# Kernel tuning notes

Hardware: AMD Instinct MI355X
Metric: run time of the kernel (lower is better)

The kernel has to match this reference:

```python
import jax, jax.numpy as jnp
import numpy as np

DIM = 256
RDIM = 64  # max(256 // 4, 16)
SCALE = RDIM ** (-0.5)
BN_EPS = 1e-5


def conv1x1(x, w):
    # x: (B, Cin, H, W), w: (Cout, Cin) -> (B, Cout, H, W)
    return jnp.einsum('bchw,oc->bohw', x, w)


def dot_attn(q, k, v):
    # q: (B, rdim, H, W); k: (B, rdim, H, W); v: (B, C, H, W)
    B, C, H, W = v.shape
    q_flat = q.reshape(B, -1, H * W).transpose(0, 2, 1)   # (B, N, rdim)
    k_flat = k.reshape(B, -1, H * W)                       # (B, rdim, N)
    v_flat = v.reshape(B, C, H * W).transpose(0, 2, 1)     # (B, N, C)
    attn = jax.nn.softmax(jnp.einsum('bnc,bcm->bnm', q_flat, k_flat) * SCALE, axis=-1)
    out = jnp.einsum('bnm,bmc->bnc', attn, v_flat)         # (B, N, C)
    return out.transpose(0, 2, 1).reshape(B, C, H, W)


def batchnorm2d(x, gamma, beta):
    # training-mode BN: stats over (B, H, W) per channel
    mean = jnp.mean(x, axis=(0, 2, 3), keepdims=True)
    var = jnp.var(x, axis=(0, 2, 3), keepdims=True)
    xn = (x - mean) * jax.lax.rsqrt(var + BN_EPS)
    return xn * gamma[None, :, None, None] + beta[None, :, None, None]


def setup_inputs() -> dict:
    key = jax.random.key(0)
    ks = jax.random.split(key, 12)
    B, H, W = 4, 64, 64
    s_q = 1.0 / np.sqrt(DIM)
    return {
        'wli_feat': jax.random.normal(ks[0], (B, DIM, H, W), jnp.float32),
        'nbi_aligned': jax.random.normal(ks[1], (B, DIM, H, W), jnp.float32),
        'w_q_wli': jax.random.normal(ks[2], (RDIM, DIM), jnp.float32) * s_q,
        'w_k_nbi': jax.random.normal(ks[3], (RDIM, DIM), jnp.float32) * s_q,
        'w_v_nbi': jax.random.normal(ks[4], (DIM, DIM), jnp.float32) * s_q,
        'w_q_nbi': jax.random.normal(ks[5], (RDIM, DIM), jnp.float32) * s_q,
        'w_k_wli': jax.random.normal(ks[6], (RDIM, DIM), jnp.float32) * s_q,
        'w_v_wli': jax.random.normal(ks[7], (DIM, DIM), jnp.float32) * s_q,
        'gamma_wli': jnp.ones((DIM,), jnp.float32),
        'beta_wli': jnp.zeros((DIM,), jnp.float32),
        'gamma_nbi': jnp.ones((DIM,), jnp.float32),
        'beta_nbi': jnp.zeros((DIM,), jnp.float32),
    }


def reference(wli_feat, nbi_aligned, w_q_wli, w_k_nbi, w_v_nbi, w_q_nbi, w_k_wli, w_v_wli,
              gamma_wli, beta_wli, gamma_nbi, beta_nbi):
    ctx_wli = dot_attn(conv1x1(wli_feat, w_q_wli), conv1x1(nbi_aligned, w_k_nbi),
                       conv1x1(nbi_aligned, w_v_nbi))
    enh_wli = batchnorm2d(wli_feat + ctx_wli, gamma_wli, beta_wli)
    ctx_nbi = dot_attn(conv1x1(nbi_aligned, w_q_nbi), conv1x1(wli_feat, w_k_wli),
                       conv1x1(wli_feat, w_v_wli))
    enh_nbi = batchnorm2d(nbi_aligned + ctx_nbi, gamma_nbi, beta_nbi)
    return enh_wli, enh_nbi
```

## Files before the change

kernel.cpp:

```cpp
#include <hip/hip_runtime.h>

#define N_TOK 4096
#define RD 64
#define CDIM 256

typedef __bf16 bf16x8 __attribute__((ext_vector_type(8)));
typedef float f32x4 __attribute__((ext_vector_type(4)));
typedef unsigned short u16;
typedef unsigned int u32;

__device__ __forceinline__ u16 f2bf(float f) {
  u32 u = __float_as_uint(f);
  u = (u + 0x7fffu + ((u >> 16) & 1u)) >> 16;
  return (u16)u;
}

__device__ __forceinline__ u32 pack2bf(float a, float b) {
  u16 ha = __builtin_bit_cast(u16, (__bf16)a);
  u16 hb = __builtin_bit_cast(u16, (__bf16)b);
  return (u32)ha | ((u32)hb << 16);
}

__device__ __forceinline__ f32x4 zero4() {
  f32x4 z = {0.f, 0.f, 0.f, 0.f};
  return z;
}

__global__ __launch_bounds__(256) void proj_kernel(
    const float* __restrict__ wli, const float* __restrict__ nbi,
    const float* __restrict__ wq0, const float* __restrict__ wk0,
    const float* __restrict__ wv0, const float* __restrict__ wq1,
    const float* __restrict__ wk1, const float* __restrict__ wv1,
    u16* __restrict__ Qb, u16* __restrict__ Kb, u16* __restrict__ Vb) {
  extern __shared__ char smem[];
  const int ntile = blockIdx.x, bb = blockIdx.y, pid = blockIdx.z;
  const int tid = threadIdx.x;
  const int w = tid >> 6, lane = tid & 63, g = lane >> 4, l15 = lane & 15;
  const int n0 = ntile * 64;

  const float* X;
  const float* W;
  u16* out;
  float scale = 1.f;
  int form, nchunk;
  switch (pid) {
    case 0: X = wli; W = wq0; out = Qb + (size_t)(0 + bb) * N_TOK * RD; scale = 0.125f; form = 1; nchunk = 1; break;
    case 1: X = nbi; W = wk0; out = Kb + (size_t)(0 + bb) * N_TOK * RD; form = 1; nchunk = 1; break;
    case 2: X = nbi; W = wv0; out = Vb + (size_t)(0 + bb) * CDIM * N_TOK; form = 2; nchunk = 4; break;
    case 3: X = nbi; W = wq1; out = Qb + (size_t)(4 + bb) * N_TOK * RD; scale = 0.125f; form = 1; nchunk = 1; break;
    case 4: X = wli; W = wk1; out = Kb + (size_t)(4 + bb) * N_TOK * RD; form = 1; nchunk = 1; break;
    default: X = wli; W = wv1; out = Vb + (size_t)(4 + bb) * CDIM * N_TOK; form = 2; nchunk = 4; break;
  }
  X += (size_t)bb * CDIM * N_TOK;

#pragma unroll
  for (int rep = 0; rep < 16; ++rep) {
    int idx = rep * 256 + tid;
    int c = idx >> 4;
    int nq = (idx & 15) * 4;
    float4 v = *(const float4*)(X + (size_t)c * N_TOK + n0 + nq);
    float vv[4] = {v.x, v.y, v.z, v.w};
#pragma unroll
    for (int k = 0; k < 4; ++k) {
      int row = nq + k;
      int addr = (row * 512 + c * 2) ^ ((row & 7) << 4);
      *(u16*)(smem + addr) = f2bf(vv[k] * scale);
    }
  }

  for (int oc = 0; oc < nchunk; ++oc) {
#pragma unroll
    for (int rep = 0; rep < 16; ++rep) {
      int idx = rep * 256 + tid;
      int o = idx >> 6;
      int c4 = (idx & 63) * 4;
      float4 v = *(const float4*)(W + (size_t)(oc * 64 + o) * CDIM + c4);
      ushort4 pk = {f2bf(v.x), f2bf(v.y), f2bf(v.z), f2bf(v.w)};
      int addr = 32768 + ((o * 512 + c4 * 2) ^ ((o & 7) << 4));
      *(ushort4*)(smem + addr) = pk;
    }
    __syncthreads();

    f32x4 acc[4];
#pragma unroll
    for (int ct = 0; ct < 4; ++ct) acc[ct] = zero4();
    const int arow = w * 16 + l15;
    const int abase = (form == 1) ? 0 : 32768;
    const int bbase = (form == 1) ? 32768 : 0;
#pragma unroll
    for (int kk = 0; kk < 8; ++kk) {
      int koff = kk * 64 + g * 16;
      bf16x8 af = *(const bf16x8*)(smem + abase + ((arow * 512 + koff) ^ ((arow & 7) << 4)));
#pragma unroll
      for (int ct = 0; ct < 4; ++ct) {
        int brow = ct * 16 + l15;
        bf16x8 bfr = *(const bf16x8*)(smem + bbase + ((brow * 512 + koff) ^ ((brow & 7) << 4)));
        acc[ct] = __builtin_amdgcn_mfma_f32_16x16x32_bf16(af, bfr, acc[ct], 0, 0, 0);
      }
    }
    if (form == 1) {
#pragma unroll
      for (int ct = 0; ct < 4; ++ct)
#pragma unroll
        for (int r = 0; r < 4; ++r)
          out[(size_t)(n0 + w * 16 + g * 4 + r) * RD + ct * 16 + l15] = f2bf(acc[ct][r]);
    } else {
#pragma unroll
      for (int ct = 0; ct < 4; ++ct)
#pragma unroll
        for (int r = 0; r < 4; ++r)
          out[(size_t)(oc * 64 + w * 16 + g * 4 + r) * N_TOK + n0 + ct * 16 + l15] = f2bf(acc[ct][r]);
    }
    __syncthreads();
  }
}

__global__ __launch_bounds__(256, 2) void attn_kernel(
    const u16* __restrict__ Qb, const u16* __restrict__ Kb,
    const u16* __restrict__ Vb, const float* __restrict__ x_wli,
    const float* __restrict__ x_nbi, float* __restrict__ y) {
  extern __shared__ char smem[];
  const int wgid = blockIdx.x;
  const int inst = wgid & 7;
  const int ntile = wgid >> 3;
  const int br = inst >> 2, bb = inst & 3;
  const int tid = threadIdx.x;
  const int w = tid >> 6, lane = tid & 63, g = lane >> 4, l15 = lane & 15;
  const u16* Q = Qb + (size_t)inst * N_TOK * RD + (size_t)ntile * 64 * RD;
  const u16* K = Kb + (size_t)inst * N_TOK * RD;
  const u16* Vt = Vb + (size_t)inst * CDIM * N_TOK;
  const float* xres = (br == 0 ? x_wli : x_nbi) + (size_t)bb * CDIM * N_TOK;
  float* yout = y + (size_t)inst * CDIM * N_TOK;

  bf16x8 qf[2];
  {
    const u16* qrow = Q + (w * 16 + l15) * RD;
    qf[0] = *(const bf16x8*)(qrow + g * 8);
    qf[1] = *(const bf16x8*)(qrow + 32 + g * 8);
  }
  f32x4 o_acc[16];
#pragma unroll
  for (int i = 0; i < 16; ++i) o_acc[i] = zero4();
  float m_ln = -1e30f, l_ln = 0.f;
  const float LOG2E = 1.44269504088896340736f;

#define STAGE_KV(kv0_, boff_)                                                    \
  {                                                                              \
    _Pragma("unroll") for (int rr = 0; rr < 2; ++rr) {                           \
      int s = w * 128 + rr * 64 + lane;                                          \
      int j = s >> 3, c16 = s & 7;                                               \
      const u16* gp = K + (size_t)((kv0_) + j) * RD + ((c16 ^ (j & 7)) * 8);     \
      char* lp = smem + (boff_) + (w * 128 + rr * 64) * 16;                      \
      __builtin_amdgcn_global_load_lds(                                          \
          (const __attribute__((address_space(1))) void*)gp,                     \
          (__attribute__((address_space(3))) void*)lp, 16, 0, 0);                \
    }                                                                            \
    _Pragma("unroll") for (int rr = 0; rr < 8; ++rr) {                           \
      int s = w * 512 + rr * 64 + lane;                                          \
      int c = s >> 3, c16 = s & 7;                                               \
      const u16* gp = Vt + (size_t)c * N_TOK + (kv0_) + ((c16 ^ (c & 7)) * 8);   \
      char* lp = smem + (boff_) + 8192 + (w * 512 + rr * 64) * 16;               \
      __builtin_amdgcn_global_load_lds(                                          \
          (const __attribute__((address_space(1))) void*)gp,                     \
          (__attribute__((address_space(3))) void*)lp, 16, 0, 0);                \
    }                                                                            \
  }

  STAGE_KV(0, 0);
  __syncthreads();

  for (int t = 0; t < 64; ++t) {
    const int kv0 = t * 64;
    const int bufOff = (t & 1) * 40960;
    if (t < 63) STAGE_KV(kv0 + 64, ((t + 1) & 1) * 40960);

    f32x4 s[4];
#pragma unroll
    for (int jt = 0; jt < 4; ++jt) {
      f32x4 acc = zero4();
#pragma unroll
      for (int kk = 0; kk < 2; ++kk) {
        int row = jt * 16 + l15;
        int addr = bufOff + ((row * 128 + kk * 64 + g * 16) ^ ((row & 7) << 4));
        bf16x8 kf = *(const bf16x8*)(smem + addr);
        acc = __builtin_amdgcn_mfma_f32_16x16x32_bf16(kf, qf[kk], acc, 0, 0, 0);
      }
      s[jt] = acc;
    }

    float mx = s[0][0];
#pragma unroll
    for (int jt = 0; jt < 4; ++jt)
#pragma unroll
      for (int r = 0; r < 4; ++r) mx = fmaxf(mx, s[jt][r]);
    mx = fmaxf(mx, __shfl_xor(mx, 16));
    mx = fmaxf(mx, __shfl_xor(mx, 32));
    if (!__all(mx - m_ln <= 8.f)) {
      float mnew = fmaxf(m_ln, mx);
      float corr = exp2f((m_ln - mnew) * LOG2E);
      m_ln = mnew;
      l_ln *= corr;
      float corrO[4];
#pragma unroll
      for (int r = 0; r < 4; ++r) corrO[r] = __shfl(corr, (lane & 48) | (g * 4 + r));
#pragma unroll
      for (int ct = 0; ct < 16; ++ct)
#pragma unroll
        for (int r = 0; r < 4; ++r) o_acc[ct][r] *= corrO[r];
    }
    float sum = 0.f;
#pragma unroll
    for (int jt = 0; jt < 4; ++jt)
#pragma unroll
      for (int r = 0; r < 4; ++r) {
        float p = exp2f((s[jt][r] - m_ln) * LOG2E);
        s[jt][r] = p;
        sum += p;
      }
    sum += __shfl_xor(sum, 16);
    sum += __shfl_xor(sum, 32);
    l_ln += sum;

    u32 pk[8];
#pragma unroll
    for (int jt = 0; jt < 4; ++jt) {
      pk[jt * 2] = pack2bf(s[jt][0], s[jt][1]);
      pk[jt * 2 + 1] = pack2bf(s[jt][2], s[jt][3]);
    }
    bf16x8 pf[2];
#pragma unroll
    for (int kk = 0; kk < 2; ++kk) {
      u32 wsel[4];
#pragma unroll
      for (int m = 0; m < 4; ++m) {
        int src = (2 * (g & 1) + (m >> 1)) * 16 + l15;
        u32 w0 = (u32)__shfl((int)pk[(2 * kk + 0) * 2 + (m & 1)], src);
        u32 w1 = (u32)__shfl((int)pk[(2 * kk + 1) * 2 + (m & 1)], src);
        wsel[m] = (g & 2) ? w1 : w0;
      }
      int4 pw = {(int)wsel[0], (int)wsel[1], (int)wsel[2], (int)wsel[3]};
      pf[kk] = __builtin_bit_cast(bf16x8, pw);
    }

    __builtin_amdgcn_s_setprio(1);
#pragma unroll
    for (int ct = 0; ct < 16; ++ct) {
      int c = ct * 16 + l15;
      int vb = bufOff + 8192;
      bf16x8 vf0 = *(const bf16x8*)(smem + vb + ((c * 128 + g * 16) ^ ((c & 7) << 4)));
      bf16x8 vf1 = *(const bf16x8*)(smem + vb + ((c * 128 + 64 + g * 16) ^ ((c & 7) << 4)));
      o_acc[ct] = __builtin_amdgcn_mfma_f32_16x16x32_bf16(pf[0], vf0, o_acc[ct], 0, 0, 0);
      o_acc[ct] = __builtin_amdgcn_mfma_f32_16x16x32_bf16(pf[1], vf1, o_acc[ct], 0, 0, 0);
    }
    __builtin_amdgcn_s_setprio(0);
    __syncthreads();
  }

  float rl = 1.f / l_ln;
  float rlO[4];
#pragma unroll
  for (int r = 0; r < 4; ++r) rlO[r] = __shfl(rl, (lane & 48) | (g * 4 + r));
  const int nbase = ntile * 64 + w * 16;
#pragma unroll
  for (int ct = 0; ct < 16; ++ct) {
    int c = ct * 16 + l15;
#pragma unroll
    for (int r = 0; r < 4; ++r) {
      size_t idx = (size_t)c * N_TOK + nbase + g * 4 + r;
      yout[idx] = xres[idx] + o_acc[ct][r] * rlO[r];
    }
  }
#undef STAGE_KV
}

__global__ __launch_bounds__(256) void bn_stats_kernel(const float* __restrict__ y,
                                                       float* __restrict__ stats) {
  const int idx = blockIdx.x;
  const int br = idx >> 8, c = idx & 255;
  const float* base = y + (size_t)br * 4 * CDIM * N_TOK + (size_t)c * N_TOK;
  float s1 = 0.f, s2 = 0.f;
#pragma unroll
  for (int bb = 0; bb < 4; ++bb) {
    const float* p = base + (size_t)bb * CDIM * N_TOK;
    for (int off = threadIdx.x * 4; off < N_TOK; off += 1024) {
      float4 v = *(const float4*)(p + off);
      s1 += v.x + v.y + v.z + v.w;
      s2 += v.x * v.x + v.y * v.y + v.z * v.z + v.w * v.w;
    }
  }
#pragma unroll
  for (int msk = 1; msk < 64; msk <<= 1) {
    s1 += __shfl_xor(s1, msk);
    s2 += __shfl_xor(s2, msk);
  }
  __shared__ float a1[4], a2[4];
  const int wv = threadIdx.x >> 6, ln = threadIdx.x & 63;
  if (ln == 0) { a1[wv] = s1; a2[wv] = s2; }
  __syncthreads();
  if (threadIdx.x == 0) {
    float t1 = a1[0] + a1[1] + a1[2] + a1[3];
    float t2 = a2[0] + a2[1] + a2[2] + a2[3];
    float mean = t1 * (1.f / 16384.f);
    float var = t2 * (1.f / 16384.f) - mean * mean;
    stats[idx] = mean;
    stats[512 + idx] = rsqrtf(var + 1e-5f);
  }
}

__global__ __launch_bounds__(256) void bn_apply_kernel(
    const float* __restrict__ y, const float* __restrict__ stats,
    const float* __restrict__ g0, const float* __restrict__ b0,
    const float* __restrict__ g1, const float* __restrict__ b1,
    float* __restrict__ out) {
  size_t i4 = (size_t)blockIdx.x * 256 + threadIdx.x;
  int br = (int)(i4 >> 20);
  int c = (int)(i4 >> 10) & 255;
  float mean = stats[br * 256 + c];
  float rstd = stats[512 + br * 256 + c];
  float ga = (br ? g1 : g0)[c];
  float be = (br ? b1 : b0)[c];
  float a = rstd * ga;
  float4 v = *(const float4*)(y + i4 * 4);
  v.x = (v.x - mean) * a + be;
  v.y = (v.y - mean) * a + be;
  v.z = (v.z - mean) * a + be;
  v.w = (v.w - mean) * a + be;
  *(float4*)(out + i4 * 4) = v;
}

extern "C" void kernel_launch(void* const* d_in, const int* in_sizes, int n_in,
                              void* d_out, int out_size, void* d_ws, size_t ws_size,
                              hipStream_t stream) {
  const float* wli = (const float*)d_in[0];
  const float* nbi = (const float*)d_in[1];
  const float* wq0 = (const float*)d_in[2];
  const float* wk0 = (const float*)d_in[3];
  const float* wv0 = (const float*)d_in[4];
  const float* wq1 = (const float*)d_in[5];
  const float* wk1 = (const float*)d_in[6];
  const float* wv1 = (const float*)d_in[7];
  const float* g0 = (const float*)d_in[8];
  const float* b0 = (const float*)d_in[9];
  const float* g1 = (const float*)d_in[10];
  const float* b1 = (const float*)d_in[11];

  char* ws = (char*)d_ws;
  u16* Qb = (u16*)(ws + 0);
  u16* Kb = (u16*)(ws + 4194304);
  u16* Vb = (u16*)(ws + 8388608);
  float* y = (float*)(ws + 25165824);
  float* stats = (float*)(ws + 58720256);

  proj_kernel<<<dim3(64, 4, 6), 256, 65536, stream>>>(wli, nbi, wq0, wk0, wv0,
                                                      wq1, wk1, wv1, Qb, Kb, Vb);
  attn_kernel<<<dim3(512), 256, 81920, stream>>>(Qb, Kb, Vb, wli, nbi, y);
  bn_stats_kernel<<<dim3(512), 256, 0, stream>>>(y, stats);
  bn_apply_kernel<<<dim3(8192), 256, 0, stream>>>(y, stats, g0, b0, g1, b1,
                                                  (float*)d_out);
}
```

Before: 301.7 us.

## Split attention waves into 2x2 query/channel tiles and drop P shuffles via 16x16x16 MFMA

Each wave now handles 32 queries and 128 output channels instead of 16 queries and 256 channels. K fragments are reused across two query tiles and V fragments across both query tiles. The P matrix is fed directly into 16x16x16 bf16 MFMAs from the QK accumulator layout, which removes the cross-lane shuffle repacking. It also adds explicit vmcnt drains before the barriers so the async LDS loads are complete, at the cost of duplicated QK and softmax work per wave pair and possibly less overlap.

After: 342.7 us. 1.14x slower.

```diff
diff --git a/kernel.cpp b/kernel.cpp
--- a/kernel.cpp
+++ b/kernel.cpp
@@ -8,6 +8,8 @@
 typedef float f32x4 __attribute__((ext_vector_type(4)));
 typedef unsigned short u16;
 typedef unsigned int u32;
+typedef u32 u32x2 __attribute__((ext_vector_type(2)));
+typedef short s16x4 __attribute__((ext_vector_type(4)));
 
 __device__ __forceinline__ u16 f2bf(float f) {
   u32 u = __float_as_uint(f);
@@ -25,6 +27,19 @@
   f32x4 z = {0.f, 0.f, 0.f, 0.f};
   return z;
 }
+
+__device__ __forceinline__ f32x4 mfma16bf(u32x2 a, u32x2 b, f32x4 c) {
+#if __has_builtin(__builtin_amdgcn_mfma_f32_16x16x16bf16_1k)
+  return __builtin_amdgcn_mfma_f32_16x16x16bf16_1k(
+      __builtin_bit_cast(s16x4, a), __builtin_bit_cast(s16x4, b), c, 0, 0, 0);
+#else
+  f32x4 d = c;
+  asm("v_mfma_f32_16x16x16_bf16 %0, %1, %2, %0" : "+v"(d) : "v"(a), "v"(b));
+  return d;
+#endif
+}
+
+#define DRAIN_VMCNT() asm volatile("s_waitcnt vmcnt(0)" ::: "memory")
 
 __global__ __launch_bounds__(256) void proj_kernel(
     const float* __restrict__ wli, const float* __restrict__ nbi,
@@ -126,29 +141,33 @@
   const int br = inst >> 2, bb = inst & 3;
   const int tid = threadIdx.x;
   const int w = tid >> 6, lane = tid & 63, g = lane >> 4, l15 = lane & 15;
+  const int wq = w >> 1, wc = w & 1;
   const u16* Q = Qb + (size_t)inst * N_TOK * RD + (size_t)ntile * 64 * RD;
   const u16* K = Kb + (size_t)inst * N_TOK * RD;
   const u16* Vt = Vb + (size_t)inst * CDIM * N_TOK;
   const float* xres = (br == 0 ? x_wli : x_nbi) + (size_t)bb * CDIM * N_TOK;
   float* yout = y + (size_t)inst * CDIM * N_TOK;
 
-  bf16x8 qf[2];
-  {
-    const u16* qrow = Q + (w * 16 + l15) * RD;
-    qf[0] = *(const bf16x8*)(qrow + g * 8);
-    qf[1] = *(const bf16x8*)(qrow + 32 + g * 8);
-  }
-  f32x4 o_acc[16];
-#pragma unroll
-  for (int i = 0; i < 16; ++i) o_acc[i] = zero4();
-  float m_ln = -1e30f, l_ln = 0.f;
+  bf16x8 qf[2][2];
+#pragma unroll
+  for (int qt = 0; qt < 2; ++qt) {
+    const u16* qrow = Q + (wq * 32 + qt * 16 + l15) * RD;
+    qf[qt][0] = *(const bf16x8*)(qrow + g * 8);
+    qf[qt][1] = *(const bf16x8*)(qrow + 32 + g * 8);
+  }
+  f32x4 o_acc[2][8];
+#pragma unroll
+  for (int qt = 0; qt < 2; ++qt)
+#pragma unroll
+    for (int ct = 0; ct < 8; ++ct) o_acc[qt][ct] = zero4();
+  float m_ln[2] = {-1e30f, -1e30f}, l_ln[2] = {0.f, 0.f};
   const float LOG2E = 1.44269504088896340736f;
 
 #define STAGE_KV(kv0_, boff_)                                                    \
   {                                                                              \
     _Pragma("unroll") for (int rr = 0; rr < 2; ++rr) {                           \
-      int s = w * 128 + rr * 64 + lane;                                          \
-      int j = s >> 3, c16 = s & 7;                                               \
+      int s_ = w * 128 + rr * 64 + lane;                                         \
+      int j = s_ >> 3, c16 = s_ & 7;                                             \
       const u16* gp = K + (size_t)((kv0_) + j) * RD + ((c16 ^ (j & 7)) * 8);     \
       char* lp = smem + (boff_) + (w * 128 + rr * 64) * 16;                      \
       __builtin_amdgcn_global_load_lds(                                          \
@@ -156,8 +175,8 @@
           (__attribute__((address_space(3))) void*)lp, 16, 0, 0);                \
     }                                                                            \
     _Pragma("unroll") for (int rr = 0; rr < 8; ++rr) {                           \
-      int s = w * 512 + rr * 64 + lane;                                          \
-      int c = s >> 3, c16 = s & 7;                                               \
+      int s_ = w * 512 + rr * 64 + lane;                                         \
+      int c = s_ >> 3, c16 = s_ & 7;                                             \
       const u16* gp = Vt + (size_t)c * N_TOK + (kv0_) + ((c16 ^ (c & 7)) * 8);   \
       char* lp = smem + (boff_) + 8192 + (w * 512 + rr * 64) * 16;               \
       __builtin_amdgcn_global_load_lds(                                          \
@@ -167,6 +186,7 @@
   }
 
   STAGE_KV(0, 0);
+  DRAIN_VMCNT();
   __syncthreads();
 
   for (int t = 0; t < 64; ++t) {
@@ -174,100 +194,111 @@
     const int bufOff = (t & 1) * 40960;
     if (t < 63) STAGE_KV(kv0 + 64, ((t + 1) & 1) * 40960);
 
-    f32x4 s[4];
+    f32x4 s[2][4];
 #pragma unroll
     for (int jt = 0; jt < 4; ++jt) {
-      f32x4 acc = zero4();
-#pragma unroll
-      for (int kk = 0; kk < 2; ++kk) {
-        int row = jt * 16 + l15;
-        int addr = bufOff + ((row * 128 + kk * 64 + g * 16) ^ ((row & 7) << 4));
-        bf16x8 kf = *(const bf16x8*)(smem + addr);
-        acc = __builtin_amdgcn_mfma_f32_16x16x32_bf16(kf, qf[kk], acc, 0, 0, 0);
-      }
-      s[jt] = acc;
-    }
-
-    float mx = s[0][0];
-#pragma unroll
-    for (int jt = 0; jt < 4; ++jt)
-#pragma unroll
-      for (int r = 0; r < 4; ++r) mx = fmaxf(mx, s[jt][r]);
-    mx = fmaxf(mx, __shfl_xor(mx, 16));
-    mx = fmaxf(mx, __shfl_xor(mx, 32));
-    if (!__all(mx - m_ln <= 8.f)) {
-      float mnew = fmaxf(m_ln, mx);
-      float corr = exp2f((m_ln - mnew) * LOG2E);
-      m_ln = mnew;
-      l_ln *= corr;
-      float corrO[4];
-#pragma unroll
-      for (int r = 0; r < 4; ++r) corrO[r] = __shfl(corr, (lane & 48) | (g * 4 + r));
-#pragma unroll
-      for (int ct = 0; ct < 16; ++ct)
-#pragma unroll
-        for (int r = 0; r < 4; ++r) o_acc[ct][r] *= corrO[r];
-    }
-    float sum = 0.f;
-#pragma unroll
-    for (int jt = 0; jt < 4; ++jt)
+      int row = jt * 16 + l15;
+      int a0 = bufOff + ((row * 128 + g * 16) ^ ((row & 7) << 4));
+      int a1 = bufOff + ((row * 128 + 64 + g * 16) ^ ((row & 7) << 4));
+      bf16x8 kf0 = *(const bf16x8*)(smem + a0);
+      bf16x8 kf1 = *(const bf16x8*)(smem + a1);
+#pragma unroll
+      for (int qt = 0; qt < 2; ++qt) {
+        f32x4 acc = __builtin_amdgcn_mfma_f32_16x16x32_bf16(kf0, qf[qt][0], zero4(), 0, 0, 0);
+        s[qt][jt] = __builtin_amdgcn_mfma_f32_16x16x32_bf16(kf1, qf[qt][1], acc, 0, 0, 0);
+      }
+    }
+
+    float mx[2];
+#pragma unroll
+    for (int qt = 0; qt < 2; ++qt) {
+      float m = s[qt][0][0];
+#pragma unroll
+      for (int jt = 0; jt < 4; ++jt)
+#pragma unroll
+        for (int r = 0; r < 4; ++r) m = fmaxf(m, s[qt][jt][r]);
+      m = fmaxf(m, __shfl_xor(m, 16));
+      m = fmaxf(m, __shfl_xor(m, 32));
+      mx[qt] = m;
+    }
+    if (!__all(mx[0] - m_ln[0] <= 8.f && mx[1] - m_ln[1] <= 8.f)) {
+#pragma unroll
+      for (int qt = 0; qt < 2; ++qt) {
+        float mnew = fmaxf(m_ln[qt], mx[qt]);
+        float corr = exp2f((m_ln[qt] - mnew) * LOG2E);
+        m_ln[qt] = mnew;
+        l_ln[qt] *= corr;
+        float corrO[4];
+#pragma unroll
+        for (int r = 0; r < 4; ++r) corrO[r] = __shfl(corr, (lane & 48) | (g * 4 + r));
+#pragma unroll
+        for (int ct = 0; ct < 8; ++ct)
+#pragma unroll
+          for (int r = 0; r < 4; ++r) o_acc[qt][ct][r] *= corrO[r];
+      }
+    }
+#pragma unroll
+    for (int qt = 0; qt < 2; ++qt) {
+      float sum = 0.f;
+#pragma unroll
+      for (int jt = 0; jt < 4; ++jt)
+#pragma unroll
+        for (int r = 0; r < 4; ++r) {
+          float p = exp2f((s[qt][jt][r] - m_ln[qt]) * LOG2E);
+          s[qt][jt][r] = p;
+          sum += p;
+        }
+      sum += __shfl_xor(sum, 16);
+      sum += __shfl_xor(sum, 32);
+      l_ln[qt] += sum;
+    }
+
+    u32x2 pa[2][4];
+#pragma unroll
+    for (int qt = 0; qt < 2; ++qt)
+#pragma unroll
+      for (int jt = 0; jt < 4; ++jt) {
+        u32x2 v;
+        v[0] = pack2bf(s[qt][jt][0], s[qt][jt][1]);
+        v[1] = pack2bf(s[qt][jt][2], s[qt][jt][3]);
+        pa[qt][jt] = v;
+      }
+
+    __builtin_amdgcn_s_setprio(1);
+    const int vb = bufOff + 8192;
+#pragma unroll
+    for (int ct = 0; ct < 8; ++ct) {
+      int c = wc * 128 + ct * 16 + l15;
+      int cbase = c * 128;
+      int cswz = (c & 7) << 4;
+#pragma unroll
+      for (int jt = 0; jt < 4; ++jt) {
+        int addr = vb + ((cbase + jt * 32 + g * 8) ^ cswz);
+        u32x2 vfr = *(const u32x2*)(smem + addr);
+        o_acc[0][ct] = mfma16bf(pa[0][jt], vfr, o_acc[0][ct]);
+        o_acc[1][ct] = mfma16bf(pa[1][jt], vfr, o_acc[1][ct]);
+      }
+    }
+    __builtin_amdgcn_s_setprio(0);
+    DRAIN_VMCNT();
+    __syncthreads();
+  }
+
+#pragma unroll
+  for (int qt = 0; qt < 2; ++qt) {
+    float rl = 1.f / l_ln[qt];
+    float rlO[4];
+#pragma unroll
+    for (int r = 0; r < 4; ++r) rlO[r] = __shfl(rl, (lane & 48) | (g * 4 + r));
+    const int nbase = ntile * 64 + wq * 32 + qt * 16;
+#pragma unroll
+    for (int ct = 0; ct < 8; ++ct) {
+      int c = wc * 128 + ct * 16 + l15;
 #pragma unroll
       for (int r = 0; r < 4; ++r) {
-        float p = exp2f((s[jt][r] - m_ln) * LOG2E);
-        s[jt][r] = p;
-        sum += p;
-      }
-    sum += __shfl_xor(sum, 16);
-    sum += __shfl_xor(sum, 32);
-    l_ln += sum;
-
-    u32 pk[8];
-#pragma unroll
-    for (int jt = 0; jt < 4; ++jt) {
-      pk[jt * 2] = pack2bf(s[jt][0], s[jt][1]);
-      pk[jt * 2 + 1] = pack2bf(s[jt][2], s[jt][3]);
-    }
-    bf16x8 pf[2];
-#pragma unroll
-    for (int kk = 0; kk < 2; ++kk) {
-      u32 wsel[4];
-#pragma unroll
-      for (int m = 0; m < 4; ++m) {
-        int src = (2 * (g & 1) + (m >> 1)) * 16 + l15;
-        u32 w0 = (u32)__shfl((int)pk[(2 * kk + 0) * 2 + (m & 1)], src);
-        u32 w1 = (u32)__shfl((int)pk[(2 * kk + 1) * 2 + (m & 1)], src);
-        wsel[m] = (g & 2) ? w1 : w0;
-      }
-      int4 pw = {(int)wsel[0], (int)wsel[1], (int)wsel[2], (int)wsel[3]};
-      pf[kk] = __builtin_bit_cast(bf16x8, pw);
-    }
-
-    __builtin_amdgcn_s_setprio(1);
-#pragma unroll
-    for (int ct = 0; ct < 16; ++ct) {
-      int c = ct * 16 + l15;
-      int vb = bufOff + 8192;
-      bf16x8 vf0 = *(const bf16x8*)(smem + vb + ((c * 128 + g * 16) ^ ((c & 7) << 4)));
-      bf16x8 vf1 = *(const bf16x8*)(smem + vb + ((c * 128 + 64 + g * 16) ^ ((c & 7) << 4)));
-      o_acc[ct] = __builtin_amdgcn_mfma_f32_16x16x32_bf16(pf[0], vf0, o_acc[ct], 0, 0, 0);
-      o_acc[ct] = __builtin_amdgcn_mfma_f32_16x16x32_bf16(pf[1], vf1, o_acc[ct], 0, 0, 0);
-    }
-    __builtin_amdgcn_s_setprio(0);
-    __syncthreads();
-  }
-
-  float rl = 1.f / l_ln;
-  float rlO[4];
-#pragma unroll
-  for (int r = 0; r < 4; ++r) rlO[r] = __shfl(rl, (lane & 48) | (g * 4 + r));
-  const int nbase = ntile * 64 + w * 16;
-#pragma unroll
-  for (int ct = 0; ct < 16; ++ct) {
-    int c = ct * 16 + l15;
-#pragma unroll
-    for (int r = 0; r < 4; ++r) {
-      size_t idx = (size_t)c * N_TOK + nbase + g * 4 + r;
-      yout[idx] = xres[idx] + o_acc[ct][r] * rlO[r];
+        size_t idx = (size_t)c * N_TOK + nbase + g * 4 + r;
+        yout[idx] = xres[idx] + o_acc[qt][ct][r] * rlO[r];
+      }
     }
   }
 #undef STAGE_KV
```
